# Optimization experiments

Measured on AMD Instinct MI355X. Metric: run time of the kernel, lower is better.

The kernel has to match this reference:

```python
import jax, jax.numpy as jnp
import numpy as np

EPS = 1e-5

def conv3(x, w, b):
    # 3x3 conv, stride 1, pad 1, NCHW/OIHW
    y = jax.lax.conv_general_dilated(x, w, (1, 1), ((1, 1), (1, 1)),
                                     dimension_numbers=('NCHW', 'OIHW', 'NCHW'))
    return y + b[None, :, None, None]

def positional_norm(x):
    # per-pixel channel-wise norm; torch .var() is unbiased (ddof=1)
    mean = jnp.mean(x, axis=1, keepdims=True)
    var = jnp.var(x, axis=1, keepdims=True, ddof=1)
    return (x - mean) / jnp.sqrt(var + EPS)

def bilinear_gather(x, py, px):
    # x: [B,C,H,W]; py/px: [B,K,H,W] absolute sample coords -> [B,C,K,H,W]
    B, C, H, W = x.shape
    K = py.shape[1]
    xf = x.reshape(B, C, H * W)
    y0 = jnp.floor(py).astype(jnp.int32)
    x0 = jnp.floor(px).astype(jnp.int32)
    wy = py - y0.astype(x.dtype)
    wx = px - x0.astype(x.dtype)

    def corner(yi, xi):
        valid = ((yi >= 0) & (yi < H) & (xi >= 0) & (xi < W)).astype(x.dtype)
        idx = (jnp.clip(yi, 0, H - 1) * W + jnp.clip(xi, 0, W - 1)).reshape(B, 1, K * H * W)
        v = jnp.take_along_axis(xf, idx, axis=2).reshape(B, C, K, H, W)
        return v * valid[:, None]

    out = ((1 - wy) * (1 - wx))[:, None] * corner(y0, x0)
    out = out + ((1 - wy) * wx)[:, None] * corner(y0, x0 + 1)
    out = out + (wy * (1 - wx))[:, None] * corner(y0 + 1, x0)
    out = out + (wy * wx)[:, None] * corner(y0 + 1, x0 + 1)
    return out

def dcn_v2(feat, cond, w_off, b_off, w_dcn, b_dcn):
    # DCNv2Pack: conv_offset(cond) -> (o1, o2, mask); modulated deformable 3x3 conv on feat
    B, C, H, W = feat.shape
    om = conv3(cond, w_off, b_off)                      # [B, 27, H, W]
    off = om[:, :18].reshape(B, 9, 2, H, W)             # (dy, dx) per kernel tap
    mask = jax.nn.sigmoid(om[:, 18:])                   # [B, 9, H, W]
    dy, dx = off[:, :, 0], off[:, :, 1]
    ki = jnp.repeat(jnp.arange(-1.0, 2.0, dtype=feat.dtype), 3)   # tap row offsets
    kj = jnp.tile(jnp.arange(-1.0, 2.0, dtype=feat.dtype), 3)     # tap col offsets
    hh = jnp.arange(H, dtype=feat.dtype)
    ww = jnp.arange(W, dtype=feat.dtype)
    py = dy + hh[None, None, :, None] + ki[None, :, None, None]
    px = dx + ww[None, None, None, :] + kj[None, :, None, None]
    sampled = bilinear_gather(feat, py, px)             # [B,C,9,H,W]
    wk = w_dcn.reshape(w_dcn.shape[0], C, 9)
    out = jnp.einsum('bkhw,bckhw,ock->bohw', mask, sampled, wk)
    return out + b_dcn[None, :, None, None]

def spade_forward(x, ref, w1, b1, w2, b2, w_off, b_off, w_dcn, b_dcn, w_g, b_g, w_be, b_be):
    normalized = positional_norm(x)
    h = jax.nn.relu(conv3(jnp.concatenate((normalized, ref), axis=1), w1, b1))
    cond = jax.nn.relu(conv3(h, w2, b2))
    ref_refine = dcn_v2(ref, cond, w_off, b_off, w_dcn, b_dcn)
    gamma = conv3(ref_refine, w_g, b_g)
    beta = conv3(ref_refine, w_be, b_be)
    return normalized * (1 + gamma) + beta

def setup_inputs() -> dict:
    key = jax.random.key(0)
    ks = jax.random.split(key, 16)
    B, NC, SC, H, W = 2, 64, 64, 96, 96
    mid = (NC + SC) // 8  # 16
    s = 0.05
    inp = {
        'x': jax.random.normal(ks[0], (B, NC, H, W), jnp.float32),
        'ref': jax.random.normal(ks[1], (B, SC, H, W), jnp.float32),
        'w1': jax.random.normal(ks[2], (mid, NC + SC, 3, 3), jnp.float32) * s,
        'b1': jax.random.normal(ks[3], (mid,), jnp.float32) * s,
        'w2': jax.random.normal(ks[4], (SC, mid, 3, 3), jnp.float32) * s,
        'b2': jax.random.normal(ks[5], (SC,), jnp.float32) * s,
        'w_off': jax.random.normal(ks[6], (27, SC, 3, 3), jnp.float32) * 0.01,
        'b_off': jax.random.normal(ks[7], (27,), jnp.float32) * 0.01,
        'w_dcn': jax.random.normal(ks[8], (SC, SC, 3, 3), jnp.float32) * s,
        'b_dcn': jax.random.normal(ks[9], (SC,), jnp.float32) * s,
        'w_g': jax.random.normal(ks[10], (NC, SC, 3, 3), jnp.float32) * s,
        'b_g': jax.random.normal(ks[11], (NC,), jnp.float32) * s,
        'w_be': jax.random.normal(ks[12], (NC, SC, 3, 3), jnp.float32) * s,
        'b_be': jax.random.normal(ks[13], (NC,), jnp.float32) * s,
    }
    return inp

def reference(x, ref, w1, b1, w2, b2, w_off, b_off, w_dcn, b_dcn, w_g, b_g, w_be, b_be):
    return spade_forward(x, ref, w1, b1, w2, b2, w_off, b_off, w_dcn, b_dcn, w_g, b_g, w_be, b_be)
```

## Files before the change

kernel.cpp:

```cpp
#include <hip/hip_runtime.h>
#include <math.h>

namespace {

typedef __attribute__((ext_vector_type(8))) short          bf16x8;
typedef __attribute__((ext_vector_type(8))) unsigned short u16x8;
typedef __attribute__((ext_vector_type(4))) float          f32x4;

constexpr int B_  = 2;
constexpr int H_  = 96;
constexpr int W_  = 96;
constexpr int HW_ = H_ * W_;
constexpr int NC_ = 64;
constexpr int SC_ = 64;

__device__ inline unsigned short f2bf(float f) {
    union { float f; unsigned u; } v; v.f = f;
    unsigned r = v.u + 0x7FFFu + ((v.u >> 16) & 1u);
    return (unsigned short)(r >> 16);
}

__device__ inline bf16x8 ld_frag(const unsigned short* p) {
    return *reinterpret_cast<const bf16x8*>(p);
}

__global__ __launch_bounds__(256)
void prep_weights(const float* __restrict__ w1, const float* __restrict__ w2,
                  const float* __restrict__ woff, const float* __restrict__ wg,
                  const float* __restrict__ wbe, const float* __restrict__ wdcn,
                  unsigned short* __restrict__ wt1, unsigned short* __restrict__ wt2,
                  unsigned short* __restrict__ wtoff, unsigned short* __restrict__ wtg,
                  unsigned short* __restrict__ wtbe, unsigned short* __restrict__ wbd) {
    int idx = blockIdx.x * 256 + threadIdx.x;
    if (idx < 9 * 16 * 128) {
        int tap = idx / (16 * 128), oc = (idx / 128) % 16, ic = idx % 128;
        wt1[idx] = f2bf(w1[(oc * 128 + ic) * 9 + tap]);
    }
    if (idx < 9 * 64 * 32) {
        int tap = idx / (64 * 32), oc = (idx / 32) % 64, ic = idx % 32;
        wt2[idx] = (ic < 16) ? f2bf(w2[(oc * 16 + ic) * 9 + tap]) : (unsigned short)0;
    }
    if (idx < 9 * 32 * 64) {
        int tap = idx / (32 * 64), oc = (idx / 64) % 32, ic = idx % 64;
        wtoff[idx] = (oc < 27) ? f2bf(woff[(oc * 64 + ic) * 9 + tap]) : (unsigned short)0;
    }
    if (idx < 9 * 64 * 64) {
        int tap = idx / (64 * 64), oc = (idx / 64) % 64, ic = idx % 64;
        wtg[idx]  = f2bf(wg [(oc * 64 + ic) * 9 + tap]);
        wtbe[idx] = f2bf(wbe[(oc * 64 + ic) * 9 + tap]);
    }
    if (idx < 64 * 576) {
        int oc = idx / 576, r = idx - oc * 576;
        int tap = r >> 6, ic = r & 63;
        wbd[idx] = f2bf(wdcn[oc * 576 + ic * 9 + tap]);
    }
}

__global__ __launch_bounds__(256)
void transpose_ref(const float* __restrict__ ref, float* __restrict__ refT,
                   unsigned short* __restrict__ cc) {
    int idx = blockIdx.x * 256 + threadIdx.x;
    if (idx >= B_ * HW_ * 16) return;
    int cg = idx & 15;
    int p  = (idx >> 4) % HW_;
    int b  = (idx >> 4) / HW_;
    const float* rb = ref + (size_t)b * SC_ * HW_ + p;
    float4 v;
    v.x = rb[(cg * 4 + 0) * HW_];
    v.y = rb[(cg * 4 + 1) * HW_];
    v.z = rb[(cg * 4 + 2) * HW_];
    v.w = rb[(cg * 4 + 3) * HW_];
    size_t bp = (size_t)b * HW_ + p;
    *reinterpret_cast<float4*>(&refT[bp * 64 + cg * 4]) = v;
    ushort4 s;
    s.x = f2bf(v.x); s.y = f2bf(v.y); s.z = f2bf(v.z); s.w = f2bf(v.w);
    *reinterpret_cast<ushort4*>(&cc[bp * 128 + 64 + cg * 4]) = s;
}

__global__ __launch_bounds__(256)
void norm_kernel(const float* __restrict__ x, float* __restrict__ nrm,
                 unsigned short* __restrict__ cc) {
    __shared__ float red1[4][64];
    __shared__ float red2[4][64];
    int blk = blockIdx.x;
    int b   = blk / 144;
    int p   = (blk % 144) * 64 + (threadIdx.x & 63);
    int cg  = threadIdx.x >> 6;

    float v[16];
    float s1 = 0.f, s2 = 0.f;
    const float* xb = x + ((size_t)b * NC_ + cg * 16) * HW_ + p;
    #pragma unroll
    for (int j = 0; j < 16; ++j) {
        v[j] = xb[j * HW_];
        s1 += v[j];
        s2 = fmaf(v[j], v[j], s2);
    }
    red1[cg][threadIdx.x & 63] = s1;
    red2[cg][threadIdx.x & 63] = s2;
    __syncthreads();
    int px = threadIdx.x & 63;
    s1 = red1[0][px] + red1[1][px] + red1[2][px] + red1[3][px];
    s2 = red2[0][px] + red2[1][px] + red2[2][px] + red2[3][px];
    float mean = s1 * (1.f / 64.f);
    float var  = (s2 - 64.f * mean * mean) * (1.f / 63.f);
    float inv  = 1.f / sqrtf(var + 1e-5f);
    float* nb = nrm + ((size_t)b * NC_ + cg * 16) * HW_ + p;
    u16x8 pk[2];
    #pragma unroll
    for (int j = 0; j < 16; ++j) {
        float nv = (v[j] - mean) * inv;
        nb[j * HW_] = nv;
        pk[j >> 3][j & 7] = f2bf(nv);
    }
    size_t bp = (size_t)b * HW_ + p;
    *reinterpret_cast<u16x8*>(&cc[bp * 128 + cg * 16 + 0]) = pk[0];
    *reinterpret_cast<u16x8*>(&cc[bp * 128 + cg * 16 + 8]) = pk[1];
}

template <int ICS, int ICP, int COLP, int COUT_PAD, int COUT_REAL,
          bool DUAL, bool RELU, bool OUTBF>
__global__ __launch_bounds__(256)
void conv_bf(const unsigned short* __restrict__ in,
             const unsigned short* __restrict__ Wt,
             const unsigned short* __restrict__ Wt2,
             const float* __restrict__ bias, const float* __restrict__ bias2,
             const float* __restrict__ nrm, float* __restrict__ outF,
             unsigned short* __restrict__ outB) {
    constexpr int NOCT = COUT_PAD / 16;
    constexpr int WPO  = 4 / NOCT;
    constexpr int MTP  = NOCT;
    constexpr int NACC = DUAL ? 2 : 1;
    constexpr int NKS  = ICP / 32;
    constexpr int NCH8 = ICP / 8;

    __shared__ unsigned short patch[6 * 18 * COLP];

    int t   = threadIdx.x;
    int blk = blockIdx.x;
    int bx  = blk % 6;
    int by  = (blk / 6) % 24;
    int b   = blk / 144;
    int x0  = bx * 16, y0 = by * 4;

    for (int e = t; e < 6 * 18 * NCH8; e += 256) {
        int kc  = e % NCH8;
        int col = (e / NCH8) % 18;
        int row = e / (NCH8 * 18);
        int yy = y0 + row - 1, xx = x0 + col - 1;
        bf16x8 v = (bf16x8){0, 0, 0, 0, 0, 0, 0, 0};
        if (kc * 8 < ICS && (unsigned)yy < (unsigned)H_ && (unsigned)xx < (unsigned)W_) {
            v = ld_frag(&in[((size_t)b * HW_ + yy * W_ + xx) * ICS + kc * 8]);
        }
        *reinterpret_cast<bf16x8*>(&patch[(row * 18 + col) * COLP + kc * 8]) = v;
    }
    __syncthreads();

    int wave = t >> 6, lane = t & 63;
    int fr = lane & 15, fq = lane >> 4;
    int oct  = wave / WPO;
    int widx = wave - oct * WPO;
    int mt0  = widx * MTP;

    f32x4 acc[MTP][NACC];
    #pragma unroll
    for (int i = 0; i < MTP; ++i)
        #pragma unroll
        for (int a = 0; a < NACC; ++a)
            acc[i][a] = (f32x4){0.f, 0.f, 0.f, 0.f};

    constexpr int dyv[9] = {0,0,0,1,1,1,2,2,2};
    constexpr int dxv[9] = {0,1,2,0,1,2,0,1,2};

    #pragma unroll
    for (int tap = 0; tap < 9; ++tap) {
        int dy = dyv[tap], dx = dxv[tap];
        #pragma unroll
        for (int ks = 0; ks < NKS; ++ks) {
            const size_t wo = ((size_t)tap * COUT_PAD + oct * 16 + fr) * ICP + ks * 32 + fq * 8;
            bf16x8 wfA = ld_frag(&Wt[wo]);
            bf16x8 wfB;
            if (DUAL) wfB = ld_frag(&Wt2[wo]);
            #pragma unroll
            for (int i = 0; i < MTP; ++i) {
                bf16x8 pf = ld_frag(&patch[((mt0 + i + dy) * 18 + (fr + dx)) * COLP
                                           + ks * 32 + fq * 8]);
                acc[i][0] = __builtin_amdgcn_mfma_f32_16x16x32_bf16(wfA, pf, acc[i][0], 0, 0, 0);
                if (DUAL)
                    acc[i][1] = __builtin_amdgcn_mfma_f32_16x16x32_bf16(wfB, pf, acc[i][1], 0, 0, 0);
            }
        }
    }

    #pragma unroll
    for (int i = 0; i < MTP; ++i) {
        int py = mt0 + i;
        if (OUTBF) {
            size_t p = (size_t)b * HW_ + (size_t)(y0 + py) * W_ + x0 + fr;
            ushort4 sv;
            #pragma unroll
            for (int j = 0; j < 4; ++j) {
                float v = acc[i][0][j] + bias[oct * 16 + fq * 4 + j];
                if (RELU) v = fmaxf(v, 0.f);
                ((unsigned short*)&sv)[j] = f2bf(v);
            }
            *reinterpret_cast<ushort4*>(&outB[p * COUT_REAL + oct * 16 + fq * 4]) = sv;
        } else {
            #pragma unroll
            for (int j = 0; j < 4; ++j) {
                int oc = oct * 16 + fq * 4 + j;
                if (oc >= COUT_REAL) continue;
                size_t off = ((size_t)b * COUT_REAL + oc) * HW_
                           + (size_t)(y0 + py) * W_ + x0 + fr;
                float v = acc[i][0][j] + bias[oc];
                if (DUAL) {
                    float be = acc[i][1][j] + bias2[oc];
                    float nv = nrm[off];
                    outF[off] = fmaf(nv, 1.f + v, be);
                } else {
                    outF[off] = RELU ? fmaxf(v, 0.f) : v;
                }
            }
        }
    }
}

constexpr int SROW = 584;

__global__ __launch_bounds__(256)
void dcn_kernel(const float* __restrict__ refT, const float* __restrict__ om,
                const unsigned short* __restrict__ wbd, const float* __restrict__ b_dcn,
                unsigned short* __restrict__ rrT) {
    __shared__ unsigned short sS[16 * SROW];
    __shared__ float4 cwL[144];
    __shared__ int4   ciL[144];

    int t  = threadIdx.x;
    int b  = blockIdx.x / 576;
    int p0 = (blockIdx.x % 576) * 16;

    const float* refb = refT + (size_t)b * HW_ * 64;
    const float* omb  = om   + (size_t)b * 27 * HW_;

    if (t < 144) {
        int pp = t / 9, k = t - pp * 9;
        int p  = p0 + pp;
        int y  = p / W_, x = p - y * W_;
        float dy = omb[(2 * k)     * HW_ + p];
        float dx = omb[(2 * k + 1) * HW_ + p];
        float mk = omb[(18 + k)    * HW_ + p];
        mk = 1.f / (1.f + expf(-mk));

        float py = dy + (float)y + (float)(k / 3 - 1);
        float px = dx + (float)x + (float)(k % 3 - 1);
        float fy = floorf(py), fx = floorf(px);
        int   y0 = (int)fy,   x0 = (int)fx;
        float wy = py - fy,   wx = px - fx;

        float cw[4];
        int   ci[4];
        #pragma unroll
        for (int i = 0; i < 4; ++i) {
            int yy = y0 + (i >> 1);
            int xx = x0 + (i & 1);
            bool valid = (yy >= 0) && (yy < H_) && (xx >= 0) && (xx < W_);
            int yc = yy < 0 ? 0 : (yy > H_ - 1 ? H_ - 1 : yy);
            int xc = xx < 0 ? 0 : (xx > W_ - 1 ? W_ - 1 : xx);
            ci[i] = yc * W_ + xc;
            float wyi = (i >> 1) ? wy : (1.f - wy);
            float wxi = (i & 1)  ? wx : (1.f - wx);
            cw[i] = valid ? mk * wyi * wxi : 0.f;
        }
        cwL[t] = make_float4(cw[0], cw[1], cw[2], cw[3]);
        ciL[t] = make_int4(ci[0], ci[1], ci[2], ci[3]);
    }
    __syncthreads();

    {
        int pp = t >> 4, cg = t & 15;
        #pragma unroll
        for (int k = 0; k < 9; ++k) {
            float4 cw = cwL[pp * 9 + k];
            int4   ci = ciL[pp * 9 + k];
            const float4 a0 = *reinterpret_cast<const float4*>(&refb[(size_t)ci.x * 64 + cg * 4]);
            const float4 a1 = *reinterpret_cast<const float4*>(&refb[(size_t)ci.y * 64 + cg * 4]);
            const float4 a2 = *reinterpret_cast<const float4*>(&refb[(size_t)ci.z * 64 + cg * 4]);
            const float4 a3 = *reinterpret_cast<const float4*>(&refb[(size_t)ci.w * 64 + cg * 4]);
            float vx = cw.x * a0.x + cw.y * a1.x + cw.z * a2.x + cw.w * a3.x;
            float vy = cw.x * a0.y + cw.y * a1.y + cw.z * a2.y + cw.w * a3.y;
            float vz = cw.x * a0.z + cw.y * a1.z + cw.z * a2.z + cw.w * a3.z;
            float vw = cw.x * a0.w + cw.y * a1.w + cw.z * a2.w + cw.w * a3.w;
            ushort4 sv;
            sv.x = f2bf(vx); sv.y = f2bf(vy); sv.z = f2bf(vz); sv.w = f2bf(vw);
            *reinterpret_cast<ushort4*>(&sS[pp * SROW + k * 64 + cg * 4]) = sv;
        }
    }
    __syncthreads();

    int wave = t >> 6, lane = t & 63;
    int fr = lane & 15, fq = lane >> 4;

    f32x4 acc = (f32x4){0.f, 0.f, 0.f, 0.f};
    for (int ks = 0; ks < 18; ++ks) {
        bf16x8 wf = ld_frag(&wbd[(size_t)(wave * 16 + fr) * 576 + ks * 32 + fq * 8]);
        bf16x8 pf = ld_frag(&sS[(size_t)fr * SROW + ks * 32 + fq * 8]);
        acc = __builtin_amdgcn_mfma_f32_16x16x32_bf16(wf, pf, acc, 0, 0, 0);
    }

    {
        size_t p = (size_t)b * HW_ + p0 + fr;
        ushort4 sv;
        #pragma unroll
        for (int j = 0; j < 4; ++j)
            ((unsigned short*)&sv)[j] = f2bf(acc[j] + b_dcn[wave * 16 + fq * 4 + j]);
        *reinterpret_cast<ushort4*>(&rrT[p * 64 + wave * 16 + fq * 4]) = sv;
    }
}

}

extern "C" void kernel_launch(void* const* d_in, const int* in_sizes, int n_in,
                              void* d_out, int out_size, void* d_ws, size_t ws_size,
                              hipStream_t stream) {
    (void)in_sizes; (void)n_in; (void)out_size; (void)ws_size;

    const float* x     = (const float*)d_in[0];
    const float* ref   = (const float*)d_in[1];
    const float* w1    = (const float*)d_in[2];
    const float* b1    = (const float*)d_in[3];
    const float* w2    = (const float*)d_in[4];
    const float* b2    = (const float*)d_in[5];
    const float* w_off = (const float*)d_in[6];
    const float* b_off = (const float*)d_in[7];
    const float* w_dcn = (const float*)d_in[8];
    const float* b_dcn = (const float*)d_in[9];
    const float* w_g   = (const float*)d_in[10];
    const float* b_g   = (const float*)d_in[11];
    const float* w_be  = (const float*)d_in[12];
    const float* b_be  = (const float*)d_in[13];

    float* out = (float*)d_out;
    float* ws  = (float*)d_ws;

    float* nrm  = ws;
    float* om   = nrm  + 1179648;
    float* refT = om   + 497664;
    unsigned short* cc    = (unsigned short*)(refT + 1179648);
    unsigned short* hmidT = cc    + 2359296;
    unsigned short* condT = hmidT + 294912;
    unsigned short* rrT   = condT + 1179648;
    unsigned short* wt1   = rrT   + 1179648;
    unsigned short* wt2   = wt1   + 18432;
    unsigned short* wtoff = wt2   + 18432;
    unsigned short* wtg   = wtoff + 18432;
    unsigned short* wtbe  = wtg   + 36864;
    unsigned short* wbd   = wtbe  + 36864;

    prep_weights<<<144, 256, 0, stream>>>(w1, w2, w_off, w_g, w_be, w_dcn,
                                          wt1, wt2, wtoff, wtg, wtbe, wbd);

    transpose_ref<<<(B_ * HW_ * 16 + 255) / 256, 256, 0, stream>>>(ref, refT, cc);

    norm_kernel<<<288, 256, 0, stream>>>(x, nrm, cc);

    constexpr int GRID = 288;

    conv_bf<128, 128, 136, 16, 16, false, true, true>
        <<<GRID, 256, 0, stream>>>(cc, wt1, nullptr, b1, nullptr, nullptr, nullptr, hmidT);

    conv_bf<16, 32, 40, 64, 64, false, true, true>
        <<<GRID, 256, 0, stream>>>(hmidT, wt2, nullptr, b2, nullptr, nullptr, nullptr, condT);

    conv_bf<64, 64, 72, 32, 27, false, false, false>
        <<<GRID, 256, 0, stream>>>(condT, wtoff, nullptr, b_off, nullptr, nullptr, om, nullptr);

    dcn_kernel<<<B_ * 576, 256, 0, stream>>>(refT, om, wbd, b_dcn, rrT);

    conv_bf<64, 64, 72, 64, 64, true, false, false>
        <<<GRID, 256, 0, stream>>>(rrT, wtg, wtbe, b_g, b_be, nrm, out, nullptr);
}
```

Before: 83.81 us.

## Fuse prologue kernels, drop fp32 refT, store offsets pixel-major for DCN

Three prologue kernels (weight prep, ref transpose, positional norm) become one launch that splits work by block index. The ref transpose now goes through a shared-memory tile, and the fp32 refT copy is gone. The DCN gather reads the bf16 ref channels already held in the concat buffer, and the offset conv writes a pixel-major [B,HW,32] layout so each DCN thread reads its offsets contiguously. This cuts two launches and some global traffic, but the bilinear gather now samples bf16 instead of fp32 ref, which lowers precision.

```diff
diff --git a/kernel.cpp b/kernel.cpp
--- a/kernel.cpp
+++ b/kernel.cpp
@@ -19,107 +19,114 @@
     unsigned r = v.u + 0x7FFFu + ((v.u >> 16) & 1u);
     return (unsigned short)(r >> 16);
 }
-
+__device__ inline float bf2f(unsigned short s) {
+    union { unsigned u; float f; } v; v.u = ((unsigned)s) << 16; return v.f;
+}
 __device__ inline bf16x8 ld_frag(const unsigned short* p) {
     return *reinterpret_cast<const bf16x8*>(p);
 }
 
 __global__ __launch_bounds__(256)
-void prep_weights(const float* __restrict__ w1, const float* __restrict__ w2,
-                  const float* __restrict__ woff, const float* __restrict__ wg,
-                  const float* __restrict__ wbe, const float* __restrict__ wdcn,
-                  unsigned short* __restrict__ wt1, unsigned short* __restrict__ wt2,
-                  unsigned short* __restrict__ wtoff, unsigned short* __restrict__ wtg,
-                  unsigned short* __restrict__ wtbe, unsigned short* __restrict__ wbd) {
-    int idx = blockIdx.x * 256 + threadIdx.x;
-    if (idx < 9 * 16 * 128) {
-        int tap = idx / (16 * 128), oc = (idx / 128) % 16, ic = idx % 128;
-        wt1[idx] = f2bf(w1[(oc * 128 + ic) * 9 + tap]);
-    }
-    if (idx < 9 * 64 * 32) {
-        int tap = idx / (64 * 32), oc = (idx / 32) % 64, ic = idx % 32;
-        wt2[idx] = (ic < 16) ? f2bf(w2[(oc * 16 + ic) * 9 + tap]) : (unsigned short)0;
-    }
-    if (idx < 9 * 32 * 64) {
-        int tap = idx / (32 * 64), oc = (idx / 64) % 32, ic = idx % 64;
-        wtoff[idx] = (oc < 27) ? f2bf(woff[(oc * 64 + ic) * 9 + tap]) : (unsigned short)0;
-    }
-    if (idx < 9 * 64 * 64) {
-        int tap = idx / (64 * 64), oc = (idx / 64) % 64, ic = idx % 64;
-        wtg[idx]  = f2bf(wg [(oc * 64 + ic) * 9 + tap]);
-        wtbe[idx] = f2bf(wbe[(oc * 64 + ic) * 9 + tap]);
-    }
-    if (idx < 64 * 576) {
-        int oc = idx / 576, r = idx - oc * 576;
-        int tap = r >> 6, ic = r & 63;
-        wbd[idx] = f2bf(wdcn[oc * 576 + ic * 9 + tap]);
-    }
-}
-
-__global__ __launch_bounds__(256)
-void transpose_ref(const float* __restrict__ ref, float* __restrict__ refT,
-                   unsigned short* __restrict__ cc) {
-    int idx = blockIdx.x * 256 + threadIdx.x;
-    if (idx >= B_ * HW_ * 16) return;
-    int cg = idx & 15;
-    int p  = (idx >> 4) % HW_;
-    int b  = (idx >> 4) / HW_;
-    const float* rb = ref + (size_t)b * SC_ * HW_ + p;
-    float4 v;
-    v.x = rb[(cg * 4 + 0) * HW_];
-    v.y = rb[(cg * 4 + 1) * HW_];
-    v.z = rb[(cg * 4 + 2) * HW_];
-    v.w = rb[(cg * 4 + 3) * HW_];
-    size_t bp = (size_t)b * HW_ + p;
-    *reinterpret_cast<float4*>(&refT[bp * 64 + cg * 4]) = v;
-    ushort4 s;
-    s.x = f2bf(v.x); s.y = f2bf(v.y); s.z = f2bf(v.z); s.w = f2bf(v.w);
-    *reinterpret_cast<ushort4*>(&cc[bp * 128 + 64 + cg * 4]) = s;
-}
-
-__global__ __launch_bounds__(256)
-void norm_kernel(const float* __restrict__ x, float* __restrict__ nrm,
-                 unsigned short* __restrict__ cc) {
+void prologue(const float* __restrict__ x, const float* __restrict__ ref,
+              const float* __restrict__ w1, const float* __restrict__ w2,
+              const float* __restrict__ woff, const float* __restrict__ wg,
+              const float* __restrict__ wbe, const float* __restrict__ wdcn,
+              float* __restrict__ nrm, unsigned short* __restrict__ cc,
+              unsigned short* __restrict__ wt1, unsigned short* __restrict__ wt2,
+              unsigned short* __restrict__ wtoff, unsigned short* __restrict__ wtg,
+              unsigned short* __restrict__ wtbe, unsigned short* __restrict__ wbd) {
     __shared__ float red1[4][64];
     __shared__ float red2[4][64];
+    __shared__ float rtile[64][65];
+
     int blk = blockIdx.x;
-    int b   = blk / 144;
-    int p   = (blk % 144) * 64 + (threadIdx.x & 63);
-    int cg  = threadIdx.x >> 6;
-
-    float v[16];
-    float s1 = 0.f, s2 = 0.f;
-    const float* xb = x + ((size_t)b * NC_ + cg * 16) * HW_ + p;
-    #pragma unroll
-    for (int j = 0; j < 16; ++j) {
-        v[j] = xb[j * HW_];
-        s1 += v[j];
-        s2 = fmaf(v[j], v[j], s2);
-    }
-    red1[cg][threadIdx.x & 63] = s1;
-    red2[cg][threadIdx.x & 63] = s2;
-    __syncthreads();
-    int px = threadIdx.x & 63;
-    s1 = red1[0][px] + red1[1][px] + red1[2][px] + red1[3][px];
-    s2 = red2[0][px] + red2[1][px] + red2[2][px] + red2[3][px];
-    float mean = s1 * (1.f / 64.f);
-    float var  = (s2 - 64.f * mean * mean) * (1.f / 63.f);
-    float inv  = 1.f / sqrtf(var + 1e-5f);
-    float* nb = nrm + ((size_t)b * NC_ + cg * 16) * HW_ + p;
-    u16x8 pk[2];
-    #pragma unroll
-    for (int j = 0; j < 16; ++j) {
-        float nv = (v[j] - mean) * inv;
-        nb[j * HW_] = nv;
-        pk[j >> 3][j & 7] = f2bf(nv);
-    }
-    size_t bp = (size_t)b * HW_ + p;
-    *reinterpret_cast<u16x8*>(&cc[bp * 128 + cg * 16 + 0]) = pk[0];
-    *reinterpret_cast<u16x8*>(&cc[bp * 128 + cg * 16 + 8]) = pk[1];
+    int t   = threadIdx.x;
+
+    if (blk < 288) {
+        int b  = blk / 144;
+        int p0 = (blk % 144) * 64;
+        int px = t & 63;
+        int cg = t >> 6;
+        int p  = p0 + px;
+
+        float v[16];
+        float s1 = 0.f, s2 = 0.f;
+        const float* xb = x + ((size_t)b * NC_ + cg * 16) * HW_ + p;
+        #pragma unroll
+        for (int j = 0; j < 16; ++j) {
+            v[j] = xb[j * HW_];
+            s1 += v[j];
+            s2 = fmaf(v[j], v[j], s2);
+        }
+        red1[cg][px] = s1;
+        red2[cg][px] = s2;
+
+        const float* rb = ref + (size_t)b * SC_ * HW_ + p0 + px;
+        #pragma unroll
+        for (int it = 0; it < 16; ++it) {
+            int ch = it * 4 + cg;
+            rtile[ch][px] = rb[(size_t)ch * HW_];
+        }
+        __syncthreads();
+
+        s1 = red1[0][px] + red1[1][px] + red1[2][px] + red1[3][px];
+        s2 = red2[0][px] + red2[1][px] + red2[2][px] + red2[3][px];
+        float mean = s1 * (1.f / 64.f);
+        float var  = (s2 - 64.f * mean * mean) * (1.f / 63.f);
+        float inv  = 1.f / sqrtf(var + 1e-5f);
+        float* nb = nrm + ((size_t)b * NC_ + cg * 16) * HW_ + p;
+        u16x8 pk[2];
+        #pragma unroll
+        for (int j = 0; j < 16; ++j) {
+            float nv = (v[j] - mean) * inv;
+            nb[j * HW_] = nv;
+            pk[j >> 3][j & 7] = f2bf(nv);
+        }
+        size_t bp = (size_t)b * HW_ + p;
+        *reinterpret_cast<u16x8*>(&cc[bp * 128 + cg * 16 + 0]) = pk[0];
+        *reinterpret_cast<u16x8*>(&cc[bp * 128 + cg * 16 + 8]) = pk[1];
+
+        {
+            int wpx = t >> 2, q = t & 3;
+            size_t bp2 = (size_t)b * HW_ + p0 + wpx;
+            u16x8 o0, o1;
+            #pragma unroll
+            for (int j = 0; j < 8; ++j) {
+                o0[j] = f2bf(rtile[q * 16 + j][wpx]);
+                o1[j] = f2bf(rtile[q * 16 + 8 + j][wpx]);
+            }
+            *reinterpret_cast<u16x8*>(&cc[bp2 * 128 + 64 + q * 16 + 0]) = o0;
+            *reinterpret_cast<u16x8*>(&cc[bp2 * 128 + 64 + q * 16 + 8]) = o1;
+        }
+    } else {
+        int idx = (blk - 288) * 256 + t;
+        if (idx < 9 * 16 * 128) {
+            int tap = idx / (16 * 128), oc = (idx / 128) % 16, ic = idx % 128;
+            wt1[idx] = f2bf(w1[(oc * 128 + ic) * 9 + tap]);
+        }
+        if (idx < 9 * 64 * 32) {
+            int tap = idx / (64 * 32), oc = (idx / 32) % 64, ic = idx % 32;
+            wt2[idx] = (ic < 16) ? f2bf(w2[(oc * 16 + ic) * 9 + tap]) : (unsigned short)0;
+        }
+        if (idx < 9 * 32 * 64) {
+            int tap = idx / (32 * 64), oc = (idx / 64) % 32, ic = idx % 64;
+            wtoff[idx] = (oc < 27) ? f2bf(woff[(oc * 64 + ic) * 9 + tap]) : (unsigned short)0;
+        }
+        if (idx < 9 * 64 * 64) {
+            int tap = idx / (64 * 64), oc = (idx / 64) % 64, ic = idx % 64;
+            wtg[idx]  = f2bf(wg [(oc * 64 + ic) * 9 + tap]);
+            wtbe[idx] = f2bf(wbe[(oc * 64 + ic) * 9 + tap]);
+        }
+        if (idx < 64 * 576) {
+            int oc = idx / 576, r = idx - oc * 576;
+            int tap = r >> 6, ic = r & 63;
+            wbd[idx] = f2bf(wdcn[oc * 576 + ic * 9 + tap]);
+        }
+    }
 }
 
 template <int ICS, int ICP, int COLP, int COUT_PAD, int COUT_REAL,
-          bool DUAL, bool RELU, bool OUTBF>
+          bool DUAL, bool RELU, int OMODE>
 __global__ __launch_bounds__(256)
 void conv_bf(const unsigned short* __restrict__ in,
              const unsigned short* __restrict__ Wt,
@@ -195,7 +202,7 @@
     #pragma unroll
     for (int i = 0; i < MTP; ++i) {
         int py = mt0 + i;
-        if (OUTBF) {
+        if (OMODE == 1) {
             size_t p = (size_t)b * HW_ + (size_t)(y0 + py) * W_ + x0 + fr;
             ushort4 sv;
             #pragma unroll
@@ -205,6 +212,16 @@
                 ((unsigned short*)&sv)[j] = f2bf(v);
             }
             *reinterpret_cast<ushort4*>(&outB[p * COUT_REAL + oct * 16 + fq * 4]) = sv;
+        } else if (OMODE == 2) {
+            size_t p = (size_t)b * HW_ + (size_t)(y0 + py) * W_ + x0 + fr;
+            float4 o4;
+            #pragma unroll
+            for (int j = 0; j < 4; ++j) {
+                int oc = oct * 16 + fq * 4 + j;
+                float v = acc[i][0][j] + (oc < COUT_REAL ? bias[oc] : 0.f);
+                ((float*)&o4)[j] = v;
+            }
+            *reinterpret_cast<float4*>(&outF[p * 32 + oct * 16 + fq * 4]) = o4;
         } else {
             #pragma unroll
             for (int j = 0; j < 4; ++j) {
@@ -228,7 +245,7 @@
 constexpr int SROW = 584;
 
 __global__ __launch_bounds__(256)
-void dcn_kernel(const float* __restrict__ refT, const float* __restrict__ om,
+void dcn_kernel(const unsigned short* __restrict__ cc, const float* __restrict__ omP,
                 const unsigned short* __restrict__ wbd, const float* __restrict__ b_dcn,
                 unsigned short* __restrict__ rrT) {
     __shared__ unsigned short sS[16 * SROW];
@@ -239,16 +256,16 @@
     int b  = blockIdx.x / 576;
     int p0 = (blockIdx.x % 576) * 16;
 
-    const float* refb = refT + (size_t)b * HW_ * 64;
-    const float* omb  = om   + (size_t)b * 27 * HW_;
+    const unsigned short* ccb = cc + (size_t)b * HW_ * 128;
 
     if (t < 144) {
         int pp = t / 9, k = t - pp * 9;
         int p  = p0 + pp;
         int y  = p / W_, x = p - y * W_;
-        float dy = omb[(2 * k)     * HW_ + p];
-        float dx = omb[(2 * k + 1) * HW_ + p];
-        float mk = omb[(18 + k)    * HW_ + p];
+        const float* omp = &omP[(size_t)(b * HW_ + p) * 32];
+        float dy = omp[2 * k];
+        float dx = omp[2 * k + 1];
+        float mk = omp[18 + k];
         mk = 1.f / (1.f + expf(-mk));
 
         float py = dy + (float)y + (float)(k / 3 - 1);
@@ -282,14 +299,14 @@
         for (int k = 0; k < 9; ++k) {
             float4 cw = cwL[pp * 9 + k];
             int4   ci = ciL[pp * 9 + k];
-            const float4 a0 = *reinterpret_cast<const float4*>(&refb[(size_t)ci.x * 64 + cg * 4]);
-            const float4 a1 = *reinterpret_cast<const float4*>(&refb[(size_t)ci.y * 64 + cg * 4]);
-            const float4 a2 = *reinterpret_cast<const float4*>(&refb[(size_t)ci.z * 64 + cg * 4]);
-            const float4 a3 = *reinterpret_cast<const float4*>(&refb[(size_t)ci.w * 64 + cg * 4]);
-            float vx = cw.x * a0.x + cw.y * a1.x + cw.z * a2.x + cw.w * a3.x;
-            float vy = cw.x * a0.y + cw.y * a1.y + cw.z * a2.y + cw.w * a3.y;
-            float vz = cw.x * a0.z + cw.y * a1.z + cw.z * a2.z + cw.w * a3.z;
-            float vw = cw.x * a0.w + cw.y * a1.w + cw.z * a2.w + cw.w * a3.w;
+            ushort4 r0 = *reinterpret_cast<const ushort4*>(&ccb[(size_t)ci.x * 128 + 64 + cg * 4]);
+            ushort4 r1 = *reinterpret_cast<const ushort4*>(&ccb[(size_t)ci.y * 128 + 64 + cg * 4]);
+            ushort4 r2 = *reinterpret_cast<const ushort4*>(&ccb[(size_t)ci.z * 128 + 64 + cg * 4]);
+            ushort4 r3 = *reinterpret_cast<const ushort4*>(&ccb[(size_t)ci.w * 128 + 64 + cg * 4]);
+            float vx = cw.x * bf2f(r0.x) + cw.y * bf2f(r1.x) + cw.z * bf2f(r2.x) + cw.w * bf2f(r3.x);
+            float vy = cw.x * bf2f(r0.y) + cw.y * bf2f(r1.y) + cw.z * bf2f(r2.y) + cw.w * bf2f(r3.y);
+            float vz = cw.x * bf2f(r0.z) + cw.y * bf2f(r1.z) + cw.z * bf2f(r2.z) + cw.w * bf2f(r3.z);
+            float vw = cw.x * bf2f(r0.w) + cw.y * bf2f(r1.w) + cw.z * bf2f(r2.w) + cw.w * bf2f(r3.w);
             ushort4 sv;
             sv.x = f2bf(vx); sv.y = f2bf(vy); sv.z = f2bf(vz); sv.w = f2bf(vw);
             *reinterpret_cast<ushort4*>(&sS[pp * SROW + k * 64 + cg * 4]) = sv;
@@ -342,10 +359,9 @@
     float* out = (float*)d_out;
     float* ws  = (float*)d_ws;
 
-    float* nrm  = ws;
-    float* om   = nrm  + 1179648;
-    float* refT = om   + 497664;
-    unsigned short* cc    = (unsigned short*)(refT + 1179648);
+    float* nrm = ws;
+    float* omP = nrm + 1179648;
+    unsigned short* cc    = (unsigned short*)(omP + 589824);
     unsigned short* hmidT = cc    + 2359296;
     unsigned short* condT = hmidT + 294912;
     unsigned short* rrT   = condT + 1179648;
@@ -356,26 +372,22 @@
     unsigned short* wtbe  = wtg   + 36864;
     unsigned short* wbd   = wtbe  + 36864;
 
-    prep_weights<<<144, 256, 0, stream>>>(w1, w2, w_off, w_g, w_be, w_dcn,
-                                          wt1, wt2, wtoff, wtg, wtbe, wbd);
-
-    transpose_ref<<<(B_ * HW_ * 16 + 255) / 256, 256, 0, stream>>>(ref, refT, cc);
-
-    norm_kernel<<<288, 256, 0, stream>>>(x, nrm, cc);
+    prologue<<<432, 256, 0, stream>>>(x, ref, w1, w2, w_off, w_g, w_be, w_dcn,
+                                      nrm, cc, wt1, wt2, wtoff, wtg, wtbe, wbd);
 
     constexpr int GRID = 288;
 
-    conv_bf<128, 128, 136, 16, 16, false, true, true>
+    conv_bf<128, 128, 136, 16, 16, false, true, 1>
         <<<GRID, 256, 0, stream>>>(cc, wt1, nullptr, b1, nullptr, nullptr, nullptr, hmidT);
 
-    conv_bf<16, 32, 40, 64, 64, false, true, true>
+    conv_bf<16, 32, 40, 64, 64, false, true, 1>
         <<<GRID, 256, 0, stream>>>(hmidT, wt2, nullptr, b2, nullptr, nullptr, nullptr, condT);
 
-    conv_bf<64, 64, 72, 32, 27, false, false, false>
-        <<<GRID, 256, 0, stream>>>(condT, wtoff, nullptr, b_off, nullptr, nullptr, om, nullptr);
-
-    dcn_kernel<<<B_ * 576, 256, 0, stream>>>(refT, om, wbd, b_dcn, rrT);
-
-    conv_bf<64, 64, 72, 64, 64, true, false, false>
+    conv_bf<64, 64, 72, 32, 27, false, false, 2>
+        <<<GRID, 256, 0, stream>>>(condT, wtoff, nullptr, b_off, nullptr, nullptr, omP, nullptr);
+
+    dcn_kernel<<<B_ * 576, 256, 0, stream>>>(cc, omP, wbd, b_dcn, rrT);
+
+    conv_bf<64, 64, 72, 64, 64, true, false, 0>
         <<<GRID, 256, 0, stream>>>(rrT, wtg, wtbe, b_g, b_be, nrm, out, nullptr);
 }
```

Measured after the change: 73.76 us. 1.14x faster.
